# Optimization experiments

Hardware: AMD Instinct MI355X
Metric: run time of the kernel (lower is better)

## Reference

```python
import math
import jax, jax.numpy as jnp
import numpy as np

B, N, M = 8, 1024, 32
D = 128      # node_dim
E = 32       # edge_dim
DD = 32      # dist_dim
MSG = 128    # message_dim
P = 128      # proj_dim
THETA = 10000.0


def _linear(x, w, b):
    return x @ w + b


def _sinusoidal(t, dim, theta=THETA):
    half = dim // 2
    freqs = jnp.exp(jnp.arange(half, dtype=t.dtype) * (-math.log(theta) / (half - 1)))
    ang = t[..., None] * freqs  # (..., half)
    return jnp.concatenate([jnp.sin(ang), jnp.cos(ang)], axis=-1)


def setup_inputs() -> dict:
    key = jax.random.key(0)
    ks = jax.random.split(key, 20)
    pair_in = 2 * D + E + DD  # NUM_ATOMS == 1

    def w(k, shape):
        fan_in = shape[0]
        return jax.random.uniform(k, shape, jnp.float32, -1, 1) / np.sqrt(fan_in)

    return {
        "embeddings": jax.random.normal(ks[0], (B, N, D), jnp.float32),
        "coords": jax.random.normal(ks[1], (B, N, 3), jnp.float32),
        "padding_mask": jnp.ones((B, N), jnp.float32),
        "edges": jax.random.normal(ks[2], (B, N, M, E), jnp.float32),
        "we_w1": w(ks[3], (pair_in, MSG)), "we_b1": jnp.zeros((MSG,), jnp.float32),
        "we_w2": w(ks[4], (MSG, MSG)),    "we_b2": jnp.zeros((MSG,), jnp.float32),
        "wx_w1": w(ks[5], (MSG, P)),      "wx_b1": jnp.zeros((P,), jnp.float32),
        "wx_w2": w(ks[6], (P, 1)),        "wx_b2": jnp.zeros((1,), jnp.float32),
        "wh_w1": w(ks[7], (D + MSG, P)),  "wh_b1": jnp.zeros((P,), jnp.float32),
        "wh_w2": w(ks[8], (P, D)),        "wh_b2": jnp.zeros((D,), jnp.float32),
        "neighbor_ids": jax.random.randint(ks[9], (B, N, M), 0, N),
    }


def _gather(x, idx):
    # x: (B, N, d), idx: (B, N, M) -> (B, N, M, d). Direct gather,
    # mathematically identical to the one-hot einsum in the original.
    Bx, Nx, d = x.shape
    flat = jnp.take_along_axis(x, idx.reshape(Bx, -1, 1), axis=1)
    return flat.reshape(Bx, Nx, idx.shape[-1], d)


def reference(embeddings, coords, padding_mask, edges,
              we_w1, we_b1, we_w2, we_b2,
              wx_w1, wx_b1, wx_w2, wx_b2,
              wh_w1, wh_b1, wh_w2, wh_b2,
              neighbor_ids):
    feats2 = _gather(embeddings, neighbor_ids)          # (B,N,M,D)
    n_coords = _gather(coords, neighbor_ids)            # (B,N,M,3)
    rel_coors = coords[:, :, None, :] - n_coords        # (B,N,M,3)
    rel_dist = jnp.linalg.norm(rel_coors, axis=-1)      # (B,N,M)
    dists = _sinusoidal(rel_dist, DD)                   # (B,N,M,DD)

    feats1 = jnp.broadcast_to(embeddings[:, :, None, :], feats2.shape)
    feats_pair = jnp.concatenate([feats1, feats2, dists, edges], axis=-1)

    h = jax.nn.relu(_linear(feats_pair, we_w1, we_b1))
    m_ij = _linear(h, we_w2, we_b2)                     # (B,N,M,MSG)

    # coordinate update (unit vectors are detached in the original)
    unit = jax.lax.stop_gradient(
        jnp.nan_to_num(rel_coors / rel_dist[..., None]))
    px = _linear(jax.nn.relu(_linear(m_ij, wx_w1, wx_b1)), wx_w2, wx_b2)
    coords_out = coords + (unit * px).sum(axis=2) / M

    # feature update
    m_masked = m_ij * padding_mask[:, :, None, None]
    m_i = m_masked.sum(axis=2) / M                      # (B,N,MSG)
    hh = jnp.concatenate([embeddings, m_i], axis=-1)
    ph = _linear(jax.nn.relu(_linear(hh, wh_w1, wh_b1)), wh_w2, wh_b2)
    embeddings_out = embeddings + ph

    return embeddings_out, coords_out
```

## Files before the change

kernel.cpp:

```cpp
#include <hip/hip_runtime.h>
#include <hip/hip_bf16.h>

typedef __hip_bfloat16 bf16;
typedef short short8 __attribute__((ext_vector_type(8)));
typedef float f32x4 __attribute__((ext_vector_type(4)));
typedef int   int4v __attribute__((ext_vector_type(4)));

#define NB 8
#define NN 1024
#define NM 32
#define ND 128
#define NE 32
#define NODES (NB*NN)
#define NPB 4

#define OFF_W1AT   0
#define OFF_W1BT   32768
#define OFF_W1CDT  65536
#define OFF_W2T    81920
#define OFF_WX1T   114688
#define OFF_WH1AT  147456
#define OFF_WH1BT  180224
#define OFF_WH2T   212992
#define OFF_Y1     245760
#define OFF_Y2     (OFF_Y1 + 2097152)
#define NEED_FAST  ((size_t)OFF_Y2 + 2097152)

__device__ __forceinline__ float toF(bf16 x){ return __bfloat162float(x); }
__device__ __forceinline__ bf16  toB(float x){ return __float2bfloat16(x); }

__device__ __forceinline__ short8 pin8(short8 w){
  union { short8 s; int4v i; } u; u.s = w;
  asm volatile("" : "+v"(u.i));
  return u.s;
}

__device__ __forceinline__ void cp16f(bf16* d, const float* s){
  #pragma unroll
  for (int q = 0; q < 4; ++q){
    float4 a = ((const float4*)s)[q];
    d[q*4+0]=toB(a.x); d[q*4+1]=toB(a.y); d[q*4+2]=toB(a.z); d[q*4+3]=toB(a.w);
  }
}
__device__ __forceinline__ void cp8f(bf16* d, const float* s){
  #pragma unroll
  for (int q = 0; q < 2; ++q){
    float4 a = ((const float4*)s)[q];
    d[q*4+0]=toB(a.x); d[q*4+1]=toB(a.y); d[q*4+2]=toB(a.z); d[q*4+3]=toB(a.w);
  }
}
__device__ __forceinline__ void cp4f(bf16* d, const float* s){
  float4 a = *(const float4*)s;
  d[0]=toB(a.x); d[1]=toB(a.y); d[2]=toB(a.z); d[3]=toB(a.w);
}

#define MFMA(a,b,c) __builtin_amdgcn_mfma_f32_16x16x32_bf16((a),(b),(c),0,0,0)

__global__ __launch_bounds__(256) void k_tr(const float* __restrict__ w1,
    const float* __restrict__ w2, const float* __restrict__ wx1,
    const float* __restrict__ wh1, const float* __restrict__ wh2,
    char* __restrict__ ws){
  int i = blockIdx.x*256 + threadIdx.x;
  const float* src; int koff, KT, dst, e;
  if      (i <  16384){ src=w1;  koff=0;   KT=128; dst=OFF_W1AT;  e=i; }
  else if (i <  32768){ src=w1;  koff=128; KT=128; dst=OFF_W1BT;  e=i-16384; }
  else if (i <  40960){ src=w1;  koff=256; KT=64;  dst=OFF_W1CDT; e=i-32768; }
  else if (i <  57344){ src=w2;  koff=0;   KT=128; dst=OFF_W2T;   e=i-40960; }
  else if (i <  73728){ src=wx1; koff=0;   KT=128; dst=OFF_WX1T;  e=i-57344; }
  else if (i <  90112){ src=wh1; koff=0;   KT=128; dst=OFF_WH1AT; e=i-73728; }
  else if (i < 106496){ src=wh1; koff=128; KT=128; dst=OFF_WH1BT; e=i-90112; }
  else if (i < 122880){ src=wh2; koff=0;   KT=128; dst=OFF_WH2T;  e=i-106496; }
  else return;
  int c = e / KT, k = e - c*KT;
  ((bf16*)(ws+dst))[e] = toB(src[(size_t)(koff+k)*128 + c]);
}

__global__ __launch_bounds__(256) void k_prep(const float* __restrict__ emb,
    const float* __restrict__ eb1, char* __restrict__ ws){
  __shared__ __align__(16) bf16 sE[32][136];
  const int tid = threadIdx.x, g0 = blockIdx.x*32;
  { const int row = tid >> 3, sub = tid & 7;
    cp16f(&sE[row][sub*16], emb + (size_t)(g0+row)*ND + sub*16); }
  __syncthreads();
  const int lane = tid & 63, wv = tid >> 6, lr = lane & 15, lk = lane >> 4;
  const int c0 = wv*16 + lr, c1 = (wv+4)*16 + lr;
  const short* wt[2] = {(const short*)(ws+OFF_W1AT), (const short*)(ws+OFF_W1BT)};
  bf16* yo[2] = {(bf16*)(ws+OFF_Y1), (bf16*)(ws+OFF_Y2)};
  #pragma unroll
  for (int t = 0; t < 2; ++t){
    f32x4 acc[2][2] = {};
    #pragma unroll
    for (int kc = 0; kc < 4; ++kc){
      const int k0 = kc*32 + lk*8;
      short8 a0 = *(const short8*)&sE[lr][k0];
      short8 a1 = *(const short8*)&sE[16+lr][k0];
      short8 w0 = *(const short8*)&wt[t][c0*128 + k0];
      short8 w1v= *(const short8*)&wt[t][c1*128 + k0];
      acc[0][0]=MFMA(a0,w0,acc[0][0]);  acc[1][0]=MFMA(a1,w0,acc[1][0]);
      acc[0][1]=MFMA(a0,w1v,acc[0][1]); acc[1][1]=MFMA(a1,w1v,acc[1][1]);
    }
    const float b0 = (t==0) ? eb1[c0] : 0.f;
    const float b1 = (t==0) ? eb1[c1] : 0.f;
    #pragma unroll
    for (int rt = 0; rt < 2; ++rt)
      #pragma unroll
      for (int r = 0; r < 4; ++r){
        const int orow = rt*16 + lk*4 + r;
        const size_t g = (size_t)(g0 + orow)*ND;
        yo[t][g + c0] = toB(acc[rt][0][r] + b0);
        yo[t][g + c1] = toB(acc[rt][1][r] + b1);
      }
  }
}

__global__ __launch_bounds__(512) void k_edges_fast(
    const float* __restrict__ coords, const float* __restrict__ mask,
    const float* __restrict__ edges,  const float* __restrict__ eb2,
    const float* __restrict__ xb1,    const float* __restrict__ xw2,
    const float* __restrict__ xb2,    const int* __restrict__ nids,
    const char* __restrict__ ws,      float* __restrict__ out)
{
  const short* w1cdT = (const short*)(ws+OFF_W1CDT);
  const short* w2T   = (const short*)(ws+OFF_W2T);
  const short* wx1T  = (const short*)(ws+OFF_WX1T);
  const bf16*  Y1    = (const bf16*)(ws+OFF_Y1);
  const bf16*  Y2    = (const bf16*)(ws+OFF_Y2);

  __shared__ __align__(16) char regA[128*136*2];
  __shared__ __align__(16) bf16 sH[128][136];
  __shared__ float sUnit[128][3];
  __shared__ float sPx[128];
  __shared__ int   sIds[128];
  bf16 (*sDE)[72]  = (bf16(*)[72])regA;
  bf16 (*sM)[136]  = (bf16(*)[136])regA;

  const int bid = blockIdx.x;
  const int nbk = ((bid & 7) << 8) + (bid >> 3);
  const int g0  = nbk * NPB;
  const int bi  = g0 >> 10;
  const int tid = threadIdx.x;
  const int lane = tid & 63, wv = tid >> 6;
  const int lr = lane & 15, lk = lane >> 4;
  const int c0 = wv*16 + lr;

  if (tid < 128) sIds[tid] = nids[(size_t)g0*NM + tid];

  short8 rw1[2], rw2[4], rwx[4];
  #pragma unroll
  for (int kc = 0; kc < 2; ++kc)
    rw1[kc] = pin8(*(const short8*)&w1cdT[c0*64 + kc*32 + lk*8]);
  #pragma unroll
  for (int kc = 0; kc < 4; ++kc){
    rw2[kc] = pin8(*(const short8*)&w2T[c0*128 + kc*32 + lk*8]);
    rwx[kc] = pin8(*(const short8*)&wx1T[c0*128 + kc*32 + lk*8]);
  }
  const float b2   = eb2[c0];
  const float bx   = xb1[c0];
  const float wx2c = xw2[c0];
  const float bx2v = xb2[0];
  float mv[NPB];
  #pragma unroll
  for (int n = 0; n < NPB; ++n) mv[n] = mask[g0+n];

  __syncthreads();

  {
    const int row = tid >> 2, sub = tid & 3;
    const int node = row >> 5;
    const int j = sIds[row];
    const float* cs = coords + (size_t)(g0+node)*3;
    const float* cj = coords + ((size_t)bi*NN + j)*3;
    const float rx = cs[0]-cj[0], ry = cs[1]-cj[1], rz = cs[2]-cj[2];
    const float d2 = rx*rx + ry*ry + rz*rz;
    const float dist = sqrtf(d2);
    if (sub == 0){
      const float inv = (d2 > 0.f) ? 1.f/dist : 0.f;
      sUnit[row][0]=rx*inv; sUnit[row][1]=ry*inv; sUnit[row][2]=rz*inv;
    }
    cp8f(&sDE[row][32 + sub*8],
         edges + ((size_t)(g0+node)*NM + (row&31))*NE + sub*8);
    #pragma unroll
    for (int q = 0; q < 8; ++q){
      const int dd = sub*8 + q, h = dd & 15;
      const float ang = dist * __expf(-0.6140226909f * (float)h);
      sDE[row][dd] = toB((dd < 16) ? __sinf(ang) : __cosf(ang));
    }
    const bf16* y1p = Y1 + (size_t)(g0+node)*ND + sub*32;
    const bf16* y2p = Y2 + ((size_t)bi*NN + j)*ND + sub*32;
    #pragma unroll
    for (int cB = 0; cB < 32; cB += 8){
      short8 a = *(const short8*)(y1p + cB);
      short8 b = *(const short8*)(y2p + cB);
      #pragma unroll
      for (int q = 0; q < 8; ++q){
        bf16 ba, bb; short sa = a[q], sb = b[q];
        __builtin_memcpy(&ba,&sa,2); __builtin_memcpy(&bb,&sb,2);
        sH[row][sub*32 + cB + q] = toB(toF(ba) + toF(bb));
      }
    }
  }
  __syncthreads();

  {
    #pragma unroll
    for (int t = 0; t < 8; ++t){
      f32x4 acc = {};
      #pragma unroll
      for (int kc = 0; kc < 2; ++kc){
        short8 a = *(const short8*)&sDE[t*16 + lr][kc*32 + lk*8];
        acc = MFMA(a, rw1[kc], acc);
      }
      #pragma unroll
      for (int r = 0; r < 4; ++r){
        const int orow = t*16 + lk*4 + r;
        sH[orow][c0] = toB(fmaxf(toF(sH[orow][c0]) + acc[r], 0.f));
      }
    }
  }
  __syncthreads();

  {
    float msum[NPB] = {};
    #pragma unroll
    for (int t = 0; t < 8; ++t){
      f32x4 acc = {};
      #pragma unroll
      for (int kc = 0; kc < 4; ++kc){
        short8 a = *(const short8*)&sH[t*16 + lr][kc*32 + lk*8];
        acc = MFMA(a, rw2[kc], acc);
      }
      #pragma unroll
      for (int r = 0; r < 4; ++r){
        const int orow = t*16 + lk*4 + r;
        const float m = acc[r] + b2;
        sM[orow][c0] = toB(m);
        msum[t>>1] += m;
      }
    }
    #pragma unroll
    for (int n = 0; n < NPB; ++n){
      msum[n] += __shfl_xor(msum[n], 16);
      msum[n] += __shfl_xor(msum[n], 32);
    }
    if (lk == 0){
      #pragma unroll
      for (int n = 0; n < NPB; ++n)
        out[(size_t)(g0+n)*ND + c0] = msum[n] * mv[n] * (1.f/32.f);
    }
  }
  __syncthreads();

  {
    #pragma unroll
    for (int t = 0; t < 8; ++t){
      f32x4 acc = {};
      #pragma unroll
      for (int kc = 0; kc < 4; ++kc){
        short8 a = *(const short8*)&sM[t*16 + lr][kc*32 + lk*8];
        acc = MFMA(a, rwx[kc], acc);
      }
      #pragma unroll
      for (int r = 0; r < 4; ++r){
        const int orow = t*16 + lk*4 + r;
        sH[orow][c0] = toB(fmaxf(acc[r] + bx, 0.f) * wx2c);
      }
    }
  }
  __syncthreads();

  {
    const int row = tid >> 2, sub = tid & 3;
    float p = 0.f;
    #pragma unroll
    for (int c8 = 0; c8 < 4; ++c8){
      short8 x = *(const short8*)&sH[row][sub*32 + c8*8];
      #pragma unroll
      for (int q = 0; q < 8; ++q){
        bf16 bq; short sq = x[q]; __builtin_memcpy(&bq,&sq,2);
        p += toF(bq);
      }
    }
    p += __shfl_xor(p, 1); p += __shfl_xor(p, 2);
    if (sub == 0) sPx[row] = p + bx2v;
  }
  __syncthreads();

  if (tid < 128){
    const float px = sPx[tid];
    float v0 = sUnit[tid][0]*px, v1 = sUnit[tid][1]*px, v2 = sUnit[tid][2]*px;
    #pragma unroll
    for (int m = 1; m < 32; m <<= 1){
      v0 += __shfl_xor(v0, m);
      v1 += __shfl_xor(v1, m);
      v2 += __shfl_xor(v2, m);
    }
    const int node = tid >> 5, d = tid & 31;
    if (d < 3){
      const float s = (d==0) ? v0 : (d==1 ? v1 : v2);
      out[(size_t)NODES*ND + (size_t)(g0+node)*3 + d] =
          coords[(size_t)(g0+node)*3 + d] + s*(1.f/32.f);
    }
  }
}

__global__ __launch_bounds__(256) void k_edges_compact(
    const float* __restrict__ emb,   const float* __restrict__ coords,
    const float* __restrict__ mask,  const float* __restrict__ edges,
    const float* __restrict__ eb1,   const float* __restrict__ eb2,
    const float* __restrict__ xb1,   const float* __restrict__ xw2,
    const float* __restrict__ xb2,   const int* __restrict__ nids,
    const char* __restrict__ ws,     float* __restrict__ out)
{
  const short* w1aT  = (const short*)(ws+OFF_W1AT);
  const short* w1bT  = (const short*)(ws+OFF_W1BT);
  const short* w1cdT = (const short*)(ws+OFF_W1CDT);
  const short* w2T   = (const short*)(ws+OFF_W2T);
  const short* wx1T  = (const short*)(ws+OFF_WX1T);

  __shared__ __align__(16) bf16 sA[32][336];
  __shared__ __align__(16) bf16 sH[32][136];
  __shared__ __align__(16) bf16 sM[32][136];
  __shared__ float sUnit[32][3];
  __shared__ float sPx[32];
  __shared__ int   sIds[32];
  __shared__ float sSelfC[3];

  const int tid = threadIdx.x;
  const int nb  = blockIdx.x;
  const int bi  = nb >> 10;

  if (tid < 32) sIds[tid] = nids[nb*NM + tid];
  if (tid < 3)  sSelfC[tid] = coords[(size_t)nb*3 + tid];
  __syncthreads();

  {
    const int row = tid >> 3, sub = tid & 7;
    const int j = sIds[row];
    cp16f(&sA[row][sub*16],       emb + (size_t)nb*ND + sub*16);
    cp16f(&sA[row][128 + sub*16], emb + ((size_t)bi*NN + j)*ND + sub*16);
    cp4f (&sA[row][288 + sub*4],  edges + ((size_t)nb*NM + row)*NE + sub*4);
    float jx = coords[((size_t)bi*NN + j)*3 + 0];
    float jy = coords[((size_t)bi*NN + j)*3 + 1];
    float jz = coords[((size_t)bi*NN + j)*3 + 2];
    float rx = sSelfC[0]-jx, ry = sSelfC[1]-jy, rz = sSelfC[2]-jz;
    float d2 = rx*rx + ry*ry + rz*rz;
    float dist = sqrtf(d2);
    if (sub == 0){
      float inv = (d2 > 0.f) ? 1.f/dist : 0.f;
      sUnit[row][0]=rx*inv; sUnit[row][1]=ry*inv; sUnit[row][2]=rz*inv;
    }
    #pragma unroll
    for (int q = 0; q < 4; ++q){
      const int dd = sub*4 + q, h = dd & 15;
      float ang = dist * __expf(-0.6140226909f * (float)h);
      sA[row][256+dd] = toB((dd < 16) ? __sinf(ang) : __cosf(ang));
    }
  }
  __syncthreads();

  const int lane = tid & 63, wv = tid >> 6, lr = lane & 15, lk = lane >> 4;
  const int c0 = wv*16 + lr, c1 = (wv+4)*16 + lr;

  {
    f32x4 acc[2][2] = {};
    #pragma unroll
    for (int kc = 0; kc < 10; ++kc){
      const int k0 = kc*32 + lk*8;
      const short* wp; int kk, KT;
      if (kc < 4){ wp = w1aT; kk = k0; KT = 128; }
      else if (kc < 8){ wp = w1bT; kk = k0-128; KT = 128; }
      else { wp = w1cdT; kk = k0-256; KT = 64; }
      short8 a0 = *(const short8*)&sA[lr][k0];
      short8 a1 = *(const short8*)&sA[16+lr][k0];
      short8 w0 = *(const short8*)&wp[c0*KT + kk];
      short8 w1v= *(const short8*)&wp[c1*KT + kk];
      acc[0][0]=MFMA(a0,w0,acc[0][0]);  acc[1][0]=MFMA(a1,w0,acc[1][0]);
      acc[0][1]=MFMA(a0,w1v,acc[0][1]); acc[1][1]=MFMA(a1,w1v,acc[1][1]);
    }
    const float b0 = eb1[c0], b1 = eb1[c1];
    #pragma unroll
    for (int rt = 0; rt < 2; ++rt)
      #pragma unroll
      for (int r = 0; r < 4; ++r){
        const int orow = rt*16 + lk*4 + r;
        sH[orow][c0] = toB(fmaxf(acc[rt][0][r]+b0, 0.f));
        sH[orow][c1] = toB(fmaxf(acc[rt][1][r]+b1, 0.f));
      }
  }
  __syncthreads();

  {
    f32x4 acc[2][2] = {};
    #pragma unroll
    for (int kc = 0; kc < 4; ++kc){
      const int k0 = kc*32 + lk*8;
      short8 a0 = *(const short8*)&sH[lr][k0];
      short8 a1 = *(const short8*)&sH[16+lr][k0];
      short8 w0 = *(const short8*)&w2T[c0*128 + k0];
      short8 w1v= *(const short8*)&w2T[c1*128 + k0];
      acc[0][0]=MFMA(a0,w0,acc[0][0]);  acc[1][0]=MFMA(a1,w0,acc[1][0]);
      acc[0][1]=MFMA(a0,w1v,acc[0][1]); acc[1][1]=MFMA(a1,w1v,acc[1][1]);
    }
    const float b0 = eb2[c0], b1 = eb2[c1];
    #pragma unroll
    for (int rt = 0; rt < 2; ++rt)
      #pragma unroll
      for (int r = 0; r < 4; ++r){
        const int orow = rt*16 + lk*4 + r;
        sM[orow][c0] = toB(acc[rt][0][r] + b0);
        sM[orow][c1] = toB(acc[rt][1][r] + b1);
      }
  }
  __syncthreads();

  {
    f32x4 acc[2][2] = {};
    #pragma unroll
    for (int kc = 0; kc < 4; ++kc){
      const int k0 = kc*32 + lk*8;
      short8 a0 = *(const short8*)&sM[lr][k0];
      short8 a1 = *(const short8*)&sM[16+lr][k0];
      short8 w0 = *(const short8*)&wx1T[c0*128 + k0];
      short8 w1v= *(const short8*)&wx1T[c1*128 + k0];
      acc[0][0]=MFMA(a0,w0,acc[0][0]);  acc[1][0]=MFMA(a1,w0,acc[1][0]);
      acc[0][1]=MFMA(a0,w1v,acc[0][1]); acc[1][1]=MFMA(a1,w1v,acc[1][1]);
    }
    const float b0 = xb1[c0], b1 = xb1[c1];
    #pragma unroll
    for (int rt = 0; rt < 2; ++rt)
      #pragma unroll
      for (int r = 0; r < 4; ++r){
        const int orow = rt*16 + lk*4 + r;
        sH[orow][c0] = toB(fmaxf(acc[rt][0][r]+b0, 0.f));
        sH[orow][c1] = toB(fmaxf(acc[rt][1][r]+b1, 0.f));
      }
  }
  __syncthreads();

  {
    const int row = tid >> 3, sub = tid & 7;
    float p = 0.f;
    #pragma unroll
    for (int q = 0; q < 16; ++q){
      const int c = sub*16 + q;
      p += toF(sH[row][c]) * xw2[c];
    }
    p += __shfl_down(p,4,8); p += __shfl_down(p,2,8); p += __shfl_down(p,1,8);
    if (sub == 0) sPx[row] = p + xb2[0];
  }
  if (tid < 128){
    float s = 0.f;
    #pragma unroll
    for (int m = 0; m < 32; ++m) s += toF(sM[m][tid]);
    out[(size_t)nb*ND + tid] = s * mask[nb] * (1.f/32.f);
  }
  __syncthreads();
  if (tid < 3){
    float s = 0.f;
    #pragma unroll
    for (int m = 0; m < 32; ++m) s += sUnit[m][tid]*sPx[m];
    out[(size_t)NODES*ND + (size_t)nb*3 + tid] = sSelfC[tid] + s*(1.f/32.f);
  }
}

__global__ __launch_bounds__(256) void k_node(
    const float* __restrict__ emb, const float* __restrict__ hb1,
    const float* __restrict__ hb2, const char* __restrict__ ws,
    float* __restrict__ out)
{
  const short* whaT = (const short*)(ws+OFF_WH1AT);
  const short* whbT = (const short*)(ws+OFF_WH1BT);
  const short* wh2T = (const short*)(ws+OFF_WH2T);
  __shared__ __align__(16) bf16 sE[32][136];
  __shared__ __align__(16) bf16 sM[32][136];
  __shared__ __align__(16) bf16 sH[32][136];
  const int tid = threadIdx.x, g0 = blockIdx.x*32;
  const int lane = tid & 63, wv = tid >> 6, lr = lane & 15, lk = lane >> 4;
  const int c0 = wv*16 + lr, c1 = (wv+4)*16 + lr;

  short8 rwa[2][4], rwb[2][4], rw2[2][4];
  #pragma unroll
  for (int kc = 0; kc < 4; ++kc){
    rwa[0][kc] = *(const short8*)&whaT[c0*128 + kc*32 + lk*8];
    rwa[1][kc] = *(const short8*)&whaT[c1*128 + kc*32 + lk*8];
    rwb[0][kc] = *(const short8*)&whbT[c0*128 + kc*32 + lk*8];
    rwb[1][kc] = *(const short8*)&whbT[c1*128 + kc*32 + lk*8];
    rw2[0][kc] = *(const short8*)&wh2T[c0*128 + kc*32 + lk*8];
    rw2[1][kc] = *(const short8*)&wh2T[c1*128 + kc*32 + lk*8];
  }
  const float b1c0 = hb1[c0], b1c1 = hb1[c1];
  const float b2c0 = hb2[c0], b2c1 = hb2[c1];

  { const int row = tid >> 3, sub = tid & 7;
    cp16f(&sE[row][sub*16], emb + (size_t)(g0+row)*ND + sub*16);
    cp16f(&sM[row][sub*16], out + (size_t)(g0+row)*ND + sub*16); }
  __syncthreads();
  {
    f32x4 acc[2][2] = {};
    #pragma unroll
    for (int kc = 0; kc < 4; ++kc){
      const int k0 = kc*32 + lk*8;
      short8 a0 = *(const short8*)&sE[lr][k0];
      short8 a1 = *(const short8*)&sE[16+lr][k0];
      acc[0][0]=MFMA(a0,rwa[0][kc],acc[0][0]); acc[1][0]=MFMA(a1,rwa[0][kc],acc[1][0]);
      acc[0][1]=MFMA(a0,rwa[1][kc],acc[0][1]); acc[1][1]=MFMA(a1,rwa[1][kc],acc[1][1]);
    }
    #pragma unroll
    for (int kc = 0; kc < 4; ++kc){
      const int k0 = kc*32 + lk*8;
      short8 a0 = *(const short8*)&sM[lr][k0];
      short8 a1 = *(const short8*)&sM[16+lr][k0];
      acc[0][0]=MFMA(a0,rwb[0][kc],acc[0][0]); acc[1][0]=MFMA(a1,rwb[0][kc],acc[1][0]);
      acc[0][1]=MFMA(a0,rwb[1][kc],acc[0][1]); acc[1][1]=MFMA(a1,rwb[1][kc],acc[1][1]);
    }
    #pragma unroll
    for (int rt = 0; rt < 2; ++rt)
      #pragma unroll
      for (int r = 0; r < 4; ++r){
        const int orow = rt*16 + lk*4 + r;
        sH[orow][c0] = toB(fmaxf(acc[rt][0][r] + b1c0, 0.f));
        sH[orow][c1] = toB(fmaxf(acc[rt][1][r] + b1c1, 0.f));
      }
  }
  __syncthreads();
  {
    f32x4 acc[2][2] = {};
    #pragma unroll
    for (int kc = 0; kc < 4; ++kc){
      const int k0 = kc*32 + lk*8;
      short8 a0 = *(const short8*)&sH[lr][k0];
      short8 a1 = *(const short8*)&sH[16+lr][k0];
      acc[0][0]=MFMA(a0,rw2[0][kc],acc[0][0]); acc[1][0]=MFMA(a1,rw2[0][kc],acc[1][0]);
      acc[0][1]=MFMA(a0,rw2[1][kc],acc[0][1]); acc[1][1]=MFMA(a1,rw2[1][kc],acc[1][1]);
    }
    #pragma unroll
    for (int rt = 0; rt < 2; ++rt)
      #pragma unroll
      for (int r = 0; r < 4; ++r){
        const int orow = rt*16 + lk*4 + r;
        const size_t g = (size_t)(g0 + orow)*ND;
        out[g + c0] = acc[rt][0][r] + b2c0 + emb[g + c0];
        out[g + c1] = acc[rt][1][r] + b2c1 + emb[g + c1];
      }
  }
}

extern "C" void kernel_launch(void* const* d_in, const int* in_sizes, int n_in,
                              void* d_out, int out_size, void* d_ws, size_t ws_size,
                              hipStream_t stream) {
  const float* emb    = (const float*)d_in[0];
  const float* coords = (const float*)d_in[1];
  const float* mask   = (const float*)d_in[2];
  const float* edges  = (const float*)d_in[3];
  const float* we_w1  = (const float*)d_in[4];
  const float* we_b1  = (const float*)d_in[5];
  const float* we_w2  = (const float*)d_in[6];
  const float* we_b2  = (const float*)d_in[7];
  const float* wx_w1  = (const float*)d_in[8];
  const float* wx_b1  = (const float*)d_in[9];
  const float* wx_w2  = (const float*)d_in[10];
  const float* wx_b2  = (const float*)d_in[11];
  const float* wh_w1  = (const float*)d_in[12];
  const float* wh_b1  = (const float*)d_in[13];
  const float* wh_w2  = (const float*)d_in[14];
  const float* wh_b2  = (const float*)d_in[15];
  const int*   nids   = (const int*)d_in[16];
  float* out = (float*)d_out;
  char* ws = (char*)d_ws;
  const bool fast = (ws_size >= NEED_FAST);

  k_tr<<<480,256,0,stream>>>(we_w1, we_w2, wx_w1, wh_w1, wh_w2, ws);

  if (fast){
    k_prep<<<NODES/32,256,0,stream>>>(emb, we_b1, ws);
    k_edges_fast<<<NODES/NPB,512,0,stream>>>(coords, mask, edges, we_b2,
        wx_b1, wx_w2, wx_b2, nids, ws, out);
  } else {
    k_edges_compact<<<NODES,256,0,stream>>>(emb, coords, mask, edges,
        we_b1, we_b2, wx_b1, wx_w2, wx_b2, nids, ws, out);
  }

  k_node<<<NODES/32,256,0,stream>>>(emb, wh_b1, wh_b2, ws, out);
}
```

Baseline: 72.90 us.

## Retile edge MLP waves to 64-row by 32-column tiles, reuse A fragments

Each wave in k_edges_fast now computes a 64-row by 32-column output tile (two column fragments) rather than all 128 rows by 16 columns. Each LDS A-fragment load now feeds two MFMAs, which halves shared-memory reads per MFMA. The sH fill is vectorized to 16-byte stores, the first-layer weights are loaded inside their stage instead of being pinned, and launch bounds now request 4 blocks per CU. The trade-off is twice as many pinned weight registers for w2 and wx1, which together with the occupancy hint could cause register spills.

```diff
diff --git a/kernel.cpp b/kernel.cpp
--- a/kernel.cpp
+++ b/kernel.cpp
@@ -13,6 +13,7 @@
 #define NE 32
 #define NODES (NB*NN)
 #define NPB 4
+#define NR  (NPB*NM)
 
 #define OFF_W1AT   0
 #define OFF_W1BT   32768
@@ -113,7 +114,7 @@
   }
 }
 
-__global__ __launch_bounds__(512) void k_edges_fast(
+__global__ __launch_bounds__(512, 4) void k_edges_fast(
     const float* __restrict__ coords, const float* __restrict__ mask,
     const float* __restrict__ edges,  const float* __restrict__ eb2,
     const float* __restrict__ xb1,    const float* __restrict__ xw2,
@@ -126,11 +127,11 @@
   const bf16*  Y1    = (const bf16*)(ws+OFF_Y1);
   const bf16*  Y2    = (const bf16*)(ws+OFF_Y2);
 
-  __shared__ __align__(16) char regA[128*136*2];
-  __shared__ __align__(16) bf16 sH[128][136];
-  __shared__ float sUnit[128][3];
-  __shared__ float sPx[128];
-  __shared__ int   sIds[128];
+  __shared__ __align__(16) char regA[NR*136*2];
+  __shared__ __align__(16) bf16 sH[NR][136];
+  __shared__ float sUnit[NR][3];
+  __shared__ float sPx[NR];
+  __shared__ int   sIds[NR];
   bf16 (*sDE)[72]  = (bf16(*)[72])regA;
   bf16 (*sM)[136]  = (bf16(*)[136])regA;
 
@@ -141,26 +142,27 @@
   const int tid = threadIdx.x;
   const int lane = tid & 63, wv = tid >> 6;
   const int lr = lane & 15, lk = lane >> 4;
-  const int c0 = wv*16 + lr;
-
-  if (tid < 128) sIds[tid] = nids[(size_t)g0*NM + tid];
-
-  short8 rw1[2], rw2[4], rwx[4];
-  #pragma unroll
-  for (int kc = 0; kc < 2; ++kc)
-    rw1[kc] = pin8(*(const short8*)&w1cdT[c0*64 + kc*32 + lk*8]);
+  const int rowhalf = wv >> 2, colq = wv & 3;
+  const int R0 = rowhalf*64;
+  const int c0 = colq*32 + lr, c1 = c0 + 16;
+
+  if (tid < NR) sIds[tid] = nids[(size_t)g0*NM + tid];
+
+  short8 rw2[2][4], rwx[2][4];
   #pragma unroll
   for (int kc = 0; kc < 4; ++kc){
-    rw2[kc] = pin8(*(const short8*)&w2T[c0*128 + kc*32 + lk*8]);
-    rwx[kc] = pin8(*(const short8*)&wx1T[c0*128 + kc*32 + lk*8]);
-  }
-  const float b2   = eb2[c0];
-  const float bx   = xb1[c0];
-  const float wx2c = xw2[c0];
-  const float bx2v = xb2[0];
-  float mv[NPB];
-  #pragma unroll
-  for (int n = 0; n < NPB; ++n) mv[n] = mask[g0+n];
+    rw2[0][kc] = pin8(*(const short8*)&w2T[c0*128 + kc*32 + lk*8]);
+    rw2[1][kc] = pin8(*(const short8*)&w2T[c1*128 + kc*32 + lk*8]);
+    rwx[0][kc] = pin8(*(const short8*)&wx1T[c0*128 + kc*32 + lk*8]);
+    rwx[1][kc] = pin8(*(const short8*)&wx1T[c1*128 + kc*32 + lk*8]);
+  }
+  const float b2c[2] = {eb2[c0], eb2[c1]};
+  const float bxc[2] = {xb1[c0], xb1[c1]};
+  const float wxc[2] = {xw2[c0], xw2[c1]};
+  const float bx2v   = xb2[0];
+  float mv[2];
+  mv[0] = mask[g0 + rowhalf*2 + 0];
+  mv[1] = mask[g0 + rowhalf*2 + 1];
 
   __syncthreads();
 
@@ -188,82 +190,107 @@
     const bf16* y1p = Y1 + (size_t)(g0+node)*ND + sub*32;
     const bf16* y2p = Y2 + ((size_t)bi*NN + j)*ND + sub*32;
     #pragma unroll
-    for (int cB = 0; cB < 32; cB += 8){
-      short8 a = *(const short8*)(y1p + cB);
-      short8 b = *(const short8*)(y2p + cB);
+    for (int h8 = 0; h8 < 4; ++h8){
+      short8 a = *(const short8*)(y1p + h8*8);
+      short8 b = *(const short8*)(y2p + h8*8);
+      short8 o;
       #pragma unroll
       for (int q = 0; q < 8; ++q){
         bf16 ba, bb; short sa = a[q], sb = b[q];
         __builtin_memcpy(&ba,&sa,2); __builtin_memcpy(&bb,&sb,2);
-        sH[row][sub*32 + cB + q] = toB(toF(ba) + toF(bb));
-      }
-    }
-  }
-  __syncthreads();
-
-  {
-    #pragma unroll
-    for (int t = 0; t < 8; ++t){
-      f32x4 acc = {};
+        bf16 rsum = toB(toF(ba) + toF(bb));
+        short sr; __builtin_memcpy(&sr,&rsum,2);
+        o[q] = sr;
+      }
+      *(short8*)&sH[row][sub*32 + h8*8] = o;
+    }
+  }
+  __syncthreads();
+
+  {
+    short8 rw1[2][2];
+    #pragma unroll
+    for (int kc = 0; kc < 2; ++kc){
+      rw1[0][kc] = *(const short8*)&w1cdT[c0*64 + kc*32 + lk*8];
+      rw1[1][kc] = *(const short8*)&w1cdT[c1*64 + kc*32 + lk*8];
+    }
+    #pragma unroll
+    for (int t = 0; t < 4; ++t){
+      f32x4 acc[2] = {};
       #pragma unroll
       for (int kc = 0; kc < 2; ++kc){
-        short8 a = *(const short8*)&sDE[t*16 + lr][kc*32 + lk*8];
-        acc = MFMA(a, rw1[kc], acc);
-      }
-      #pragma unroll
-      for (int r = 0; r < 4; ++r){
-        const int orow = t*16 + lk*4 + r;
-        sH[orow][c0] = toB(fmaxf(toF(sH[orow][c0]) + acc[r], 0.f));
-      }
-    }
-  }
-  __syncthreads();
-
-  {
-    float msum[NPB] = {};
-    #pragma unroll
-    for (int t = 0; t < 8; ++t){
-      f32x4 acc = {};
+        short8 a = *(const short8*)&sDE[R0 + t*16 + lr][kc*32 + lk*8];
+        acc[0] = MFMA(a, rw1[0][kc], acc[0]);
+        acc[1] = MFMA(a, rw1[1][kc], acc[1]);
+      }
+      #pragma unroll
+      for (int p = 0; p < 2; ++p)
+        #pragma unroll
+        for (int r = 0; r < 4; ++r){
+          const int orow = R0 + t*16 + lk*4 + r;
+          const int cc = p ? c1 : c0;
+          sH[orow][cc] = toB(fmaxf(toF(sH[orow][cc]) + acc[p][r], 0.f));
+        }
+    }
+  }
+  __syncthreads();
+
+  {
+    float msum[2][2] = {};
+    #pragma unroll
+    for (int t = 0; t < 4; ++t){
+      f32x4 acc[2] = {};
       #pragma unroll
       for (int kc = 0; kc < 4; ++kc){
-        short8 a = *(const short8*)&sH[t*16 + lr][kc*32 + lk*8];
-        acc = MFMA(a, rw2[kc], acc);
-      }
-      #pragma unroll
-      for (int r = 0; r < 4; ++r){
-        const int orow = t*16 + lk*4 + r;
-        const float m = acc[r] + b2;
-        sM[orow][c0] = toB(m);
-        msum[t>>1] += m;
-      }
-    }
-    #pragma unroll
-    for (int n = 0; n < NPB; ++n){
-      msum[n] += __shfl_xor(msum[n], 16);
-      msum[n] += __shfl_xor(msum[n], 32);
-    }
+        short8 a = *(const short8*)&sH[R0 + t*16 + lr][kc*32 + lk*8];
+        acc[0] = MFMA(a, rw2[0][kc], acc[0]);
+        acc[1] = MFMA(a, rw2[1][kc], acc[1]);
+      }
+      #pragma unroll
+      for (int p = 0; p < 2; ++p)
+        #pragma unroll
+        for (int r = 0; r < 4; ++r){
+          const int orow = R0 + t*16 + lk*4 + r;
+          const float m = acc[p][r] + b2c[p];
+          sM[orow][p ? c1 : c0] = toB(m);
+          msum[p][t>>1] += m;
+        }
+    }
+    #pragma unroll
+    for (int p = 0; p < 2; ++p)
+      #pragma unroll
+      for (int n = 0; n < 2; ++n){
+        msum[p][n] += __shfl_xor(msum[p][n], 16);
+        msum[p][n] += __shfl_xor(msum[p][n], 32);
+      }
     if (lk == 0){
       #pragma unroll
-      for (int n = 0; n < NPB; ++n)
-        out[(size_t)(g0+n)*ND + c0] = msum[n] * mv[n] * (1.f/32.f);
-    }
-  }
-  __syncthreads();
-
-  {
-    #pragma unroll
-    for (int t = 0; t < 8; ++t){
-      f32x4 acc = {};
+      for (int n = 0; n < 2; ++n){
+        const size_t gq = (size_t)(g0 + rowhalf*2 + n)*ND;
+        out[gq + c0] = msum[0][n] * mv[n] * (1.f/32.f);
+        out[gq + c1] = msum[1][n] * mv[n] * (1.f/32.f);
+      }
+    }
+  }
+  __syncthreads();
+
+  {
+    #pragma unroll
+    for (int t = 0; t < 4; ++t){
+      f32x4 acc[2] = {};
       #pragma unroll
       for (int kc = 0; kc < 4; ++kc){
-        short8 a = *(const short8*)&sM[t*16 + lr][kc*32 + lk*8];
-        acc = MFMA(a, rwx[kc], acc);
-      }
-      #pragma unroll
-      for (int r = 0; r < 4; ++r){
-        const int orow = t*16 + lk*4 + r;
-        sH[orow][c0] = toB(fmaxf(acc[r] + bx, 0.f) * wx2c);
-      }
+        short8 a = *(const short8*)&sM[R0 + t*16 + lr][kc*32 + lk*8];
+        acc[0] = MFMA(a, rwx[0][kc], acc[0]);
+        acc[1] = MFMA(a, rwx[1][kc], acc[1]);
+      }
+      #pragma unroll
+      for (int p = 0; p < 2; ++p)
+        #pragma unroll
+        for (int r = 0; r < 4; ++r){
+          const int orow = R0 + t*16 + lk*4 + r;
+          sH[orow][p ? c1 : c0] = toB(fmaxf(acc[p][r] + bxc[p], 0.f) * wxc[p]);
+        }
     }
   }
   __syncthreads();
@@ -285,7 +312,7 @@
   }
   __syncthreads();
 
-  if (tid < 128){
+  if (tid < NR){
     const float px = sPx[tid];
     float v0 = sUnit[tid][0]*px, v1 = sUnit[tid][1]*px, v2 = sUnit[tid][2]*px;
     #pragma unroll
```

Result: slower. 81.75 us (+12.1%).
